# Optimization experiments

Hardware: AMD Instinct MI355X
Metric: run time of the kernel (lower is better)

## Reference

```python
import jax, jax.numpy as jnp
import numpy as np

CH_IN = 64
CH_OUT = 64
KSIZE = 2
DILATION = 1
HID = 32


def _conv1x1(z, w, b):
    # z: [B, Cin, K], w: [Cout, Cin], b: [Cout] -> [B, Cout, K]
    return jnp.einsum('oi,bik->bok', w, z) + b[None, :, None]


def setup_inputs() -> dict:
    key = jax.random.key(0)
    ks = jax.random.split(key, 10)
    B, T, K, ZDIM = 8, 65536, 1024, 128
    s = 0.05
    return {
        'x': jax.random.normal(ks[0], (B, CH_IN, T), jnp.float32),
        'z': jax.random.normal(ks[1], (B, ZDIM, K), jnp.float32),
        'w1': jax.random.normal(ks[2], (HID, ZDIM), jnp.float32) * s,
        'b1': jax.random.normal(ks[3], (HID,), jnp.float32) * s,
        'w2': jax.random.normal(ks[4], (CH_IN * CH_OUT * KSIZE, HID), jnp.float32) * s,
        'b2': jax.random.normal(ks[5], (CH_IN * CH_OUT * KSIZE,), jnp.float32) * s,
        'w3': jax.random.normal(ks[6], (HID, ZDIM), jnp.float32) * s,
        'b3': jax.random.normal(ks[7], (HID,), jnp.float32) * s,
        'w4': jax.random.normal(ks[8], (CH_OUT, HID), jnp.float32) * s,
        'b4': jax.random.normal(ks[9], (CH_OUT,), jnp.float32) * s,
    }


def reference(x, z, w1, b1, w2, b2, w3, b3, w4, b4):
    B, _, T = x.shape
    K = z.shape[-1]
    S = T // K  # samples per conditioning step
    pad = DILATION * (KSIZE - 1)
    xp = jnp.pad(x, ((0, 0), (0, 0), (pad, 0)))
    # unfold: concat shifted copies along channel dim -> [B, CH_IN*KSIZE, T]
    xu = jnp.concatenate(
        [xp[:, :, pad - i * DILATION: pad - i * DILATION + T] for i in range(KSIZE)],
        axis=1)
    # [B*K, S, CH_IN*KSIZE]
    xr = xu.transpose(0, 2, 1).reshape(B * K, S, CH_IN * KSIZE)
    # hyper-generated weights: [B, CH_IN*KSIZE*CH_OUT, K]
    wfeat = _conv1x1(jax.nn.relu(_conv1x1(z, w1, b1)), w2, b2)
    weight = wfeat.reshape(B, CH_IN * KSIZE, CH_OUT, K).transpose(0, 3, 1, 2)
    weight = weight.reshape(B * K, CH_IN * KSIZE, CH_OUT)
    # hyper-generated bias: [B*K, CH_OUT]
    bfeat = _conv1x1(jax.nn.relu(_conv1x1(z, w3, b3)), w4, b4)  # [B, CH_OUT, K]
    bias = bfeat.transpose(0, 2, 1).reshape(B * K, CH_OUT)
    # batched matmul + bias
    y = jnp.einsum('nsc,nco->nso', xr, weight) + bias[:, None, :]
    return y.reshape(B, T, CH_OUT).transpose(0, 2, 1)
```

## Files before the change

### kernel.cpp

```cpp
#include <hip/hip_runtime.h>
#include <hip/hip_bf16.h>

#define CIN   64
#define COUT  64
#define HID   32
#define ZD    128
#define KC    1024
#define SPC   64
#define TLEN  65536

typedef __attribute__((ext_vector_type(8))) short bf16x8;
typedef __attribute__((ext_vector_type(4))) float f32x4;

__device__ __forceinline__ unsigned f2bf(float f) {
    unsigned u = __float_as_uint(f);
    unsigned r = u + 0x7fffu + ((u >> 16) & 1u);
    return r >> 16;
}
__device__ __forceinline__ unsigned pk2(float a, float b) {
    return f2bf(a) | (f2bf(b) << 16);
}

__global__ void cast_w2_kernel(const float* __restrict__ w2, unsigned* __restrict__ w2b) {
    int i  = blockIdx.x * 256 + threadIdx.x;
    int r  = i >> 4;
    int hp = i & 15;
    w2b[i] = pk2(w2[r * HID + 2 * hp], w2[r * HID + 2 * hp + 1]);
}

__global__ __launch_bounds__(256, 2)
void hyperconv_mfma(const float* __restrict__ x, const float* __restrict__ z,
                    const float* __restrict__ w1, const float* __restrict__ b1,
                    const float* __restrict__ b2,
                    const float* __restrict__ w3, const float* __restrict__ b3,
                    const float* __restrict__ w4, const float* __restrict__ b4,
                    const uint4* __restrict__ w2b,
                    float* __restrict__ out)
{
    __shared__ float s_z[4][ZD];
    __shared__ float s_h3[4][HID];
    __shared__ float s_bias[4][COUT];
    __shared__ __align__(16) short s_h1b[4][HID];
    __shared__ __align__(16) short s_w[4][8192];

    const int tid  = threadIdx.x;
    const int w    = tid >> 6;
    const int lane = tid & 63;
    const int l15  = lane & 15;
    const int q    = lane >> 4;
    const int n0   = blockIdx.x * 4;
    const int b    = n0 >> 10;
    const int kk0  = n0 & 1023;

    #pragma unroll
    for (int i = 0; i < 2; ++i) {
        int idx = tid + i * 256;
        int g = idx >> 7, d = idx & 127;
        s_z[g][d] = z[((size_t)b * ZD + d) * KC + kk0 + g];
    }
    __syncthreads();

    {
        int g = tid >> 6, u = tid & 63;
        const float* wrow = (u < HID) ? (w1 + u * ZD) : (w3 + (u - HID) * ZD);
        float acc = (u < HID) ? b1[u] : b3[u - HID];
        #pragma unroll
        for (int d4 = 0; d4 < ZD / 4; ++d4) {
            float4 wv = *(const float4*)(wrow + 4 * d4);
            float4 zv = *(const float4*)(&s_z[g][4 * d4]);
            acc += wv.x * zv.x + wv.y * zv.y + wv.z * zv.z + wv.w * zv.w;
        }
        acc = fmaxf(acc, 0.f);
        if (u < HID) s_h1b[g][u] = (short)f2bf(acc);
        else         s_h3[g][u - HID] = acc;
    }
    __syncthreads();

    {
        int g = tid >> 6, o = tid & 63;
        float acc = b4[o];
        #pragma unroll
        for (int h4 = 0; h4 < HID / 4; ++h4) {
            float4 wv = *(const float4*)(w4 + o * HID + 4 * h4);
            float4 hv = *(const float4*)(&s_h3[g][4 * h4]);
            acc += wv.x * hv.x + wv.y * hv.y + wv.z * hv.z + wv.w * hv.w;
        }
        s_bias[g][o] = acc;
    }

    {
        bf16x8 afrag = *(const bf16x8*)&s_h1b[l15 & 3][q * 8];
        const int rb = w * 2048;
        #pragma unroll
        for (int ntl = 0; ntl < 4; ++ntl) {
            #pragma unroll
            for (int q2 = 0; q2 < 4; ++q2) {
                float cv[4][8];
                #pragma unroll
                for (int jj = 0; jj < 8; ++jj) {
                    int r = rb + 512 * q2 + 64 * jj + 16 * ntl + l15;
                    bf16x8 bfrag = __builtin_bit_cast(bf16x8, w2b[r * 4 + q]);
                    f32x4 c = __builtin_amdgcn_mfma_f32_16x16x32_bf16(
                        afrag, bfrag, (f32x4){0.f, 0.f, 0.f, 0.f}, 0, 0, 0);
                    float b2v = b2[r];
                    #pragma unroll
                    for (int reg = 0; reg < 4; ++reg) cv[reg][jj] = c[reg] + b2v;
                }
                if (lane < 16) {
                    #pragma unroll
                    for (int reg = 0; reg < 4; ++reg) {
                        uint4 res;
                        res.x = pk2(cv[reg][0], cv[reg][1]);
                        res.y = pk2(cv[reg][2], cv[reg][3]);
                        res.z = pk2(cv[reg][4], cv[reg][5]);
                        res.w = pk2(cv[reg][6], cv[reg][7]);
                        *(uint4*)&s_w[reg][rb + 512 * q2 + (16 * ntl + l15) * 8] = res;
                    }
                }
            }
        }
    }
    __syncthreads();

    {
        const int t0 = (kk0 + w) * SPC;
        const float* xb = x + (size_t)b * CIN * TLEN;
        f32x4 acc[4][4];
        #pragma unroll
        for (int i = 0; i < 4; ++i)
            #pragma unroll
            for (int j = 0; j < 4; ++j) acc[i][j] = (f32x4){0.f, 0.f, 0.f, 0.f};

        for (int ks = 0; ks < 4; ++ks) {
            bf16x8 afr[4];
            #pragma unroll
            for (int ot = 0; ot < 4; ++ot)
                afr[ot] = *(const bf16x8*)&s_w[w][ks * 2048 + q * 512 + (16 * ot + l15) * 8];

            const int koff = (ks >= 2) ? -1 : 0;
            const int c0 = (ks & 1) * 32 + 8 * q;
            bf16x8 bfr[4];
            #pragma unroll
            for (int st = 0; st < 4; ++st) {
                int t = t0 + 16 * st + l15 + koff;
                int tc = t < 0 ? 0 : t;
                float v[8];
                #pragma unroll
                for (int j = 0; j < 8; ++j)
                    v[j] = xb[(size_t)(c0 + j) * TLEN + tc];
                if (t < 0) {
                    #pragma unroll
                    for (int j = 0; j < 8; ++j) v[j] = 0.f;
                }
                uint4 p;
                p.x = pk2(v[0], v[1]); p.y = pk2(v[2], v[3]);
                p.z = pk2(v[4], v[5]); p.w = pk2(v[6], v[7]);
                bfr[st] = __builtin_bit_cast(bf16x8, p);
            }

            #pragma unroll
            for (int ot = 0; ot < 4; ++ot)
                #pragma unroll
                for (int st = 0; st < 4; ++st)
                    acc[ot][st] = __builtin_amdgcn_mfma_f32_16x16x32_bf16(
                        afr[ot], bfr[st], acc[ot][st], 0, 0, 0);
        }

        float* ob = out + (size_t)b * COUT * TLEN;
        #pragma unroll
        for (int ot = 0; ot < 4; ++ot) {
            f32x4 bv = *(const f32x4*)&s_bias[w][16 * ot + 4 * q];
            #pragma unroll
            for (int st = 0; st < 4; ++st) {
                int t = t0 + 16 * st + l15;
                #pragma unroll
                for (int reg = 0; reg < 4; ++reg)
                    ob[(size_t)(16 * ot + 4 * q + reg) * TLEN + t] = acc[ot][st][reg] + bv[reg];
            }
        }
    }
}

extern "C" void kernel_launch(void* const* d_in, const int* in_sizes, int n_in,
                              void* d_out, int out_size, void* d_ws, size_t ws_size,
                              hipStream_t stream) {
    const float* x  = (const float*)d_in[0];
    const float* z  = (const float*)d_in[1];
    const float* w1 = (const float*)d_in[2];
    const float* b1 = (const float*)d_in[3];
    const float* w2 = (const float*)d_in[4];
    const float* b2 = (const float*)d_in[5];
    const float* w3 = (const float*)d_in[6];
    const float* b3 = (const float*)d_in[7];
    const float* w4 = (const float*)d_in[8];
    const float* b4 = (const float*)d_in[9];
    float* out = (float*)d_out;
    unsigned* w2b = (unsigned*)d_ws;

    cast_w2_kernel<<<512, 256, 0, stream>>>(w2, w2b);
    hyperconv_mfma<<<2048, 256, 0, stream>>>(x, z, w1, b1, b2, w3, b3, w4, b4,
                                             (const uint4*)w2b, out);
}
```

Before: 362.3 us.

## Pre-transpose x to bf16 and double-buffer hypernetwork weight generation

Adds a pre-pass that casts x to bf16 and transposes it to time-major order, so the main kernel fetches one 16-byte vector per MFMA fragment instead of eight strided fp32 loads. The hyper-weight generation is split into four K-slices written into a smaller double-buffered LDS array and interleaved with the main MFMA loop. Bias b2 is folded into the MFMA accumulator, and launch bounds are raised to target four blocks per CU. The cost is an extra full pass over x (read fp32, write bf16) plus a workspace dependency, with a fallback path when the workspace is too small.

After: 413.8 us. 14.2% more time.

```diff
diff --git a/kernel.cpp b/kernel.cpp
--- a/kernel.cpp
+++ b/kernel.cpp
@@ -1,5 +1,4 @@
 #include <hip/hip_runtime.h>
-#include <hip/hip_bf16.h>
 
 #define CIN   64
 #define COUT  64
@@ -28,8 +27,36 @@
     w2b[i] = pk2(w2[r * HID + 2 * hp], w2[r * HID + 2 * hp + 1]);
 }
 
-__global__ __launch_bounds__(256, 2)
-void hyperconv_mfma(const float* __restrict__ x, const float* __restrict__ z,
+__global__ __launch_bounds__(256)
+void transpose_cast_x(const float* __restrict__ x, unsigned short* __restrict__ xT) {
+    __shared__ unsigned short s[64][66];
+    const int blk  = blockIdx.x;
+    const int b    = blk >> 10;
+    const int t0   = (blk & 1023) << 6;
+    const int lane = threadIdx.x & 63;
+    const int wv   = threadIdx.x >> 6;
+    const float* xb = x + (size_t)b * CIN * TLEN;
+    #pragma unroll
+    for (int cc = 0; cc < 16; ++cc) {
+        int c = cc * 4 + wv;
+        s[lane][c] = (unsigned short)f2bf(xb[(size_t)c * TLEN + t0 + lane]);
+    }
+    __syncthreads();
+    unsigned short* ob = xT + ((size_t)b * TLEN + t0) * CIN;
+    #pragma unroll
+    for (int half = 0; half < 2; ++half) {
+        int si = (half * 256 + threadIdx.x) * 8;
+        int t = si >> 6, c = si & 63;
+        const unsigned* sp = (const unsigned*)&s[t][c];
+        uint4 v; v.x = sp[0]; v.y = sp[1]; v.z = sp[2]; v.w = sp[3];
+        *(uint4*)&ob[(size_t)t * CIN + c] = v;
+    }
+}
+
+template<bool USE_XT>
+__global__ __launch_bounds__(256, 4)
+void hyperconv_mfma(const float* __restrict__ x, const unsigned short* __restrict__ xT,
+                    const float* __restrict__ z,
                     const float* __restrict__ w1, const float* __restrict__ b1,
                     const float* __restrict__ b2,
                     const float* __restrict__ w3, const float* __restrict__ b3,
@@ -37,11 +64,11 @@
                     const uint4* __restrict__ w2b,
                     float* __restrict__ out)
 {
-    __shared__ float s_z[4][ZD];
-    __shared__ float s_h3[4][HID];
-    __shared__ float s_bias[4][COUT];
+    __shared__ __align__(16) float s_z[4][ZD];
+    __shared__ __align__(16) float s_h3[4][HID];
+    __shared__ __align__(16) float s_bias[4][COUT];
     __shared__ __align__(16) short s_h1b[4][HID];
-    __shared__ __align__(16) short s_w[4][8192];
+    __shared__ __align__(16) short s_wc[2][4][2048];
 
     const int tid  = threadIdx.x;
     const int w    = tid >> 6;
@@ -88,58 +115,65 @@
         s_bias[g][o] = acc;
     }
 
-    {
-        bf16x8 afrag = *(const bf16x8*)&s_h1b[l15 & 3][q * 8];
-        const int rb = w * 2048;
+    bf16x8 afrag = *(const bf16x8*)&s_h1b[l15 >> 2][q * 8];
+
+    auto produce = [&](int ksr, int buf) {
+        const int rb = ksr * 2048 + w * 512;
         #pragma unroll
         for (int ntl = 0; ntl < 4; ++ntl) {
-            #pragma unroll
-            for (int q2 = 0; q2 < 4; ++q2) {
-                float cv[4][8];
-                #pragma unroll
-                for (int jj = 0; jj < 8; ++jj) {
-                    int r = rb + 512 * q2 + 64 * jj + 16 * ntl + l15;
-                    bf16x8 bfrag = __builtin_bit_cast(bf16x8, w2b[r * 4 + q]);
-                    f32x4 c = __builtin_amdgcn_mfma_f32_16x16x32_bf16(
-                        afrag, bfrag, (f32x4){0.f, 0.f, 0.f, 0.f}, 0, 0, 0);
-                    float b2v = b2[r];
-                    #pragma unroll
-                    for (int reg = 0; reg < 4; ++reg) cv[reg][jj] = c[reg] + b2v;
-                }
-                if (lane < 16) {
-                    #pragma unroll
-                    for (int reg = 0; reg < 4; ++reg) {
-                        uint4 res;
-                        res.x = pk2(cv[reg][0], cv[reg][1]);
-                        res.y = pk2(cv[reg][2], cv[reg][3]);
-                        res.z = pk2(cv[reg][4], cv[reg][5]);
-                        res.w = pk2(cv[reg][6], cv[reg][7]);
-                        *(uint4*)&s_w[reg][rb + 512 * q2 + (16 * ntl + l15) * 8] = res;
-                    }
-                }
+            float cvq[8];
+            #pragma unroll
+            for (int jj = 0; jj < 8; ++jj) {
+                int r = rb + 64 * jj + 16 * ntl + l15;
+                float b2v = b2[r];
+                bf16x8 bfrag = __builtin_bit_cast(bf16x8, w2b[r * 4 + q]);
+                f32x4 c = __builtin_amdgcn_mfma_f32_16x16x32_bf16(
+                    afrag, bfrag, (f32x4){b2v, b2v, b2v, b2v}, 0, 0, 0);
+                cvq[jj] = c[0];
             }
-        }
-    }
-    __syncthreads();
-
-    {
-        const int t0 = (kk0 + w) * SPC;
-        const float* xb = x + (size_t)b * CIN * TLEN;
-        f32x4 acc[4][4];
-        #pragma unroll
-        for (int i = 0; i < 4; ++i)
-            #pragma unroll
-            for (int j = 0; j < 4; ++j) acc[i][j] = (f32x4){0.f, 0.f, 0.f, 0.f};
-
-        for (int ks = 0; ks < 4; ++ks) {
-            bf16x8 afr[4];
-            #pragma unroll
-            for (int ot = 0; ot < 4; ++ot)
-                afr[ot] = *(const bf16x8*)&s_w[w][ks * 2048 + q * 512 + (16 * ot + l15) * 8];
-
-            const int koff = (ks >= 2) ? -1 : 0;
-            const int c0 = (ks & 1) * 32 + 8 * q;
-            bf16x8 bfr[4];
+            uint4 res;
+            res.x = pk2(cvq[0], cvq[1]);
+            res.y = pk2(cvq[2], cvq[3]);
+            res.z = pk2(cvq[4], cvq[5]);
+            res.w = pk2(cvq[6], cvq[7]);
+            *(uint4*)&s_wc[buf][q][w * 512 + (16 * ntl + l15) * 8] = res;
+        }
+    };
+
+    produce(0, 0);
+    __syncthreads();
+
+    const int t0 = (kk0 + w) * SPC;
+    const float* xb = x + (size_t)b * CIN * TLEN;
+    const unsigned short* xtb = xT + (size_t)b * TLEN * CIN;
+
+    f32x4 acc[4][4];
+    #pragma unroll
+    for (int i = 0; i < 4; ++i)
+        #pragma unroll
+        for (int j = 0; j < 4; ++j) acc[i][j] = (f32x4){0.f, 0.f, 0.f, 0.f};
+
+    #pragma unroll
+    for (int ks = 0; ks < 4; ++ks) {
+        const int buf = ks & 1;
+
+        bf16x8 afr[4];
+        #pragma unroll
+        for (int ot = 0; ot < 4; ++ot)
+            afr[ot] = *(const bf16x8*)&s_wc[buf][w][q * 512 + (16 * ot + l15) * 8];
+
+        const int koff = (ks >= 2) ? -1 : 0;
+        const int c0 = (ks & 1) * 32 + 8 * q;
+        bf16x8 bfr[4];
+        if (USE_XT) {
+            #pragma unroll
+            for (int st = 0; st < 4; ++st) {
+                int t = t0 + 16 * st + l15 + koff;
+                uint4 p = (uint4){0u, 0u, 0u, 0u};
+                if (t >= 0) p = *(const uint4*)&xtb[(size_t)t * CIN + c0];
+                bfr[st] = __builtin_bit_cast(bf16x8, p);
+            }
+        } else {
             #pragma unroll
             for (int st = 0; st < 4; ++st) {
                 int t = t0 + 16 * st + l15 + koff;
@@ -157,26 +191,30 @@
                 p.z = pk2(v[4], v[5]); p.w = pk2(v[6], v[7]);
                 bfr[st] = __builtin_bit_cast(bf16x8, p);
             }
-
-            #pragma unroll
-            for (int ot = 0; ot < 4; ++ot)
-                #pragma unroll
-                for (int st = 0; st < 4; ++st)
-                    acc[ot][st] = __builtin_amdgcn_mfma_f32_16x16x32_bf16(
-                        afr[ot], bfr[st], acc[ot][st], 0, 0, 0);
-        }
-
-        float* ob = out + (size_t)b * COUT * TLEN;
-        #pragma unroll
-        for (int ot = 0; ot < 4; ++ot) {
-            f32x4 bv = *(const f32x4*)&s_bias[w][16 * ot + 4 * q];
-            #pragma unroll
-            for (int st = 0; st < 4; ++st) {
-                int t = t0 + 16 * st + l15;
-                #pragma unroll
-                for (int reg = 0; reg < 4; ++reg)
-                    ob[(size_t)(16 * ot + 4 * q + reg) * TLEN + t] = acc[ot][st][reg] + bv[reg];
-            }
+        }
+
+        if (ks < 3) produce(ks + 1, buf ^ 1);
+
+        #pragma unroll
+        for (int ot = 0; ot < 4; ++ot)
+            #pragma unroll
+            for (int st = 0; st < 4; ++st)
+                acc[ot][st] = __builtin_amdgcn_mfma_f32_16x16x32_bf16(
+                    afr[ot], bfr[st], acc[ot][st], 0, 0, 0);
+
+        if (ks < 3) __syncthreads();
+    }
+
+    float* ob = out + (size_t)b * COUT * TLEN;
+    #pragma unroll
+    for (int ot = 0; ot < 4; ++ot) {
+        f32x4 bv = *(const f32x4*)&s_bias[w][16 * ot + 4 * q];
+        #pragma unroll
+        for (int st = 0; st < 4; ++st) {
+            int t = t0 + 16 * st + l15;
+            #pragma unroll
+            for (int reg = 0; reg < 4; ++reg)
+                ob[(size_t)(16 * ot + 4 * q + reg) * TLEN + t] = acc[ot][st][reg] + bv[reg];
         }
     }
 }
@@ -195,9 +233,18 @@
     const float* w4 = (const float*)d_in[8];
     const float* b4 = (const float*)d_in[9];
     float* out = (float*)d_out;
+
     unsigned* w2b = (unsigned*)d_ws;
+    unsigned short* xT = (unsigned short*)((char*)d_ws + 524288);
+    const size_t need_xt = 524288ull + (size_t)8 * TLEN * CIN * 2;
 
     cast_w2_kernel<<<512, 256, 0, stream>>>(w2, w2b);
-    hyperconv_mfma<<<2048, 256, 0, stream>>>(x, z, w1, b1, b2, w3, b3, w4, b4,
-                                             (const uint4*)w2b, out);
-}
+    if (ws_size >= need_xt) {
+        transpose_cast_x<<<8192, 256, 0, stream>>>(x, xT);
+        hyperconv_mfma<true><<<2048, 256, 0, stream>>>(x, xT, z, w1, b1, b2, w3, b3, w4, b4,
+                                                       (const uint4*)w2b, out);
+    } else {
+        hyperconv_mfma<false><<<2048, 256, 0, stream>>>(x, xT, z, w1, b1, b2, w3, b3, w4, b4,
+                                                        (const uint4*)w2b, out);
+    }
+}
```
